# Optimization experiments

Hardware: AMD Instinct MI355X
Metric: run time of the kernel (lower is better)

The kernel has to match this reference:

```python
import math
import jax, jax.numpy as jnp
import numpy as np

B, S, D, H, FF, L = 2, 1024, 1024, 16, 4096, 4
HD = D // H
EPS = 1e-5


def setup_inputs() -> dict:
    key = jax.random.key(0)
    ks = jax.random.split(key, 14)
    sd = 0.02
    inp = {
        "x": jax.random.normal(ks[0], (B, S, D), jnp.float32),
        "mask": jnp.zeros((S, S), jnp.float32),
        "Wqkv": jax.random.normal(ks[1], (L, D, 3 * D), jnp.float32) * sd,
        "bqkv": jnp.zeros((L, 3 * D), jnp.float32),
        "Wo": jax.random.normal(ks[2], (L, D, D), jnp.float32) * sd,
        "bo": jnp.zeros((L, D), jnp.float32),
        "g1": jnp.ones((L, D), jnp.float32),
        "be1": jnp.zeros((L, D), jnp.float32),
        "W1": jax.random.normal(ks[3], (L, D, FF), jnp.float32) * sd,
        "bf1": jnp.zeros((L, FF), jnp.float32),
        "W2": jax.random.normal(ks[4], (L, FF, D), jnp.float32) * sd,
        "bf2": jnp.zeros((L, D), jnp.float32),
        "g2": jnp.ones((L, D), jnp.float32),
        "be2": jnp.zeros((L, D), jnp.float32),
    }
    return inp


def _layer_norm(x, g, b):
    # biased variance, matching the torch LayerNormalization module
    mean = jnp.mean(x, axis=-1, keepdims=True)
    var = jnp.mean((x - mean) ** 2, axis=-1, keepdims=True)
    return g * (x - mean) / jnp.sqrt(var + EPS) + b


def _encoder(x, mask, params):
    inv_sqrt_dk = 1.0 / math.sqrt(HD)

    def step(h, p):
        Wqkv, bqkv, Wo, bo, g1, be1, W1, bf1, W2, bf2, g2, be2 = p
        b, s, d = h.shape
        qkv = h @ Wqkv + bqkv                         # [B,S,3D]
        qkv = qkv.reshape(b, s, H, 3 * HD).transpose(0, 2, 1, 3)  # [B,H,S,3hd]
        q, k, v = jnp.split(qkv, 3, axis=-1)          # each [B,H,S,hd]
        scores = jnp.einsum("bhqd,bhkd->bhqk", q, k) * inv_sqrt_dk + mask
        attn = jax.nn.softmax(scores, axis=-1)
        vals = jnp.einsum("bhqk,bhkd->bhqd", attn, v)
        vals = vals.transpose(0, 2, 1, 3).reshape(b, s, d)
        a = vals @ Wo + bo
        h = _layer_norm(h + a, g1, be1)
        f = jax.nn.relu(h @ W1 + bf1) @ W2 + bf2
        h = _layer_norm(h + f, g2, be2)
        return h, None

    out, _ = jax.lax.scan(step, x, params)
    return out


def reference(x, mask, Wqkv, bqkv, Wo, bo, g1, be1, W1, bf1, W2, bf2, g2, be2):
    params = (Wqkv, bqkv, Wo, bo, g1, be1, W1, bf1, W2, bf2, g2, be2)
    return _encoder(x, mask, params)
```

## Files before the change

kernel.cpp:

```cpp
#include <hip/hip_runtime.h>
#include <hip/hip_bf16.h>
#include <cmath>

typedef __attribute__((ext_vector_type(8))) short short8;
typedef __attribute__((ext_vector_type(4))) float f32x4;

#define EPI_QKV 0
#define EPI_RELU 2
#define EPI_PART 3

__device__ __forceinline__ void gl2lds16(const void* g, void* l) {
  __builtin_amdgcn_global_load_lds(
      (const __attribute__((address_space(1))) unsigned int*)g,
      (__attribute__((address_space(3))) unsigned int*)l, 16, 0, 0);
}

template <int EPI>
__global__ __launch_bounds__(256) void gemm_k(
    const __hip_bfloat16* __restrict__ A, const __hip_bfloat16* __restrict__ WT,
    const float* __restrict__ bias, float* __restrict__ outF,
    __hip_bfloat16* __restrict__ outB, __hip_bfloat16* __restrict__ Qo,
    __hip_bfloat16* __restrict__ Ko, __hip_bfloat16* __restrict__ VTo, int M,
    int N, int K, int P) {
  __shared__ __align__(16) __hip_bfloat16 Alds[128 * 32];
  __shared__ __align__(16) __hip_bfloat16 Blds[128 * 32];
  const int tid = threadIdx.x;
  const int nbn = N >> 7;
  const int npb = (M >> 7) * nbn;
  const int nwg = gridDim.x;
  const int cpx = nwg >> 3;
  const int bid = blockIdx.x;
  const int wg = (bid & 7) * cpx + (bid >> 3);
  const int part = wg / npb;
  const int wgl = wg - part * npb;
  const int bm = wgl / nbn, bn = wgl - bm * nbn;
  const int brow = bm << 7, bcol = bn << 7;
  const int lane = tid & 63;
  const int wid = tid >> 6;
  const int wm = wid >> 1, wn = wid & 1;
  const int lr = lane & 15, lk = lane >> 4;
  const int Kp = K / P;
  const int k0 = part * Kp;

  f32x4 acc[4][4] = {};

  const int srow = tid >> 2;
  const int ssw = (tid >> 3) & 3;
  const int scol = (((tid & 3) ^ ssw) << 3);
  const __hip_bfloat16* aptr = A + (size_t)(brow + srow) * K + scol + k0;
  const __hip_bfloat16* bptr = WT + (size_t)(bcol + srow) * K + scol + k0;
  __hip_bfloat16* la = &Alds[tid * 8];
  __hip_bfloat16* lb = &Blds[tid * 8];
  const size_t K64 = (size_t)64 * K;
  const int fsw = (lr >> 1) & 3;

  for (int kt = 0; kt < Kp; kt += 32) {
    gl2lds16(aptr + kt, la);
    gl2lds16(aptr + K64 + kt, la + 2048);
    gl2lds16(bptr + kt, lb);
    gl2lds16(bptr + K64 + kt, lb + 2048);
    __syncthreads();
    short8 af[4], bf[4];
#pragma unroll
    for (int m = 0; m < 4; ++m)
      af[m] = *(const short8*)&Alds[(wm * 64 + m * 16 + lr) * 32 + ((lk ^ fsw) << 3)];
#pragma unroll
    for (int n = 0; n < 4; ++n)
      bf[n] = *(const short8*)&Blds[(wn * 64 + n * 16 + lr) * 32 + ((lk ^ fsw) << 3)];
#pragma unroll
    for (int m = 0; m < 4; ++m)
#pragma unroll
      for (int n = 0; n < 4; ++n)
        acc[m][n] =
            __builtin_amdgcn_mfma_f32_16x16x32_bf16(af[m], bf[n], acc[m][n], 0, 0, 0);
    __syncthreads();
  }

#pragma unroll
  for (int n = 0; n < 4; ++n) {
    const int c = bcol + wn * 64 + n * 16 + lr;
    float bb = 0.f;
    if constexpr (EPI != EPI_PART) bb = bias[c];
#pragma unroll
    for (int m = 0; m < 4; ++m) {
#pragma unroll
      for (int r = 0; r < 4; ++r) {
        const int row = brow + wm * 64 + m * 16 + lk * 4 + r;
        float v = acc[m][n][r] + bb;
        if constexpr (EPI == EPI_PART) {
          outF[((size_t)part * M + row) * N + c] = v;
        } else if constexpr (EPI == EPI_RELU) {
          outB[(size_t)row * N + c] = __float2bfloat16(fmaxf(v, 0.f));
        } else {
          const int b = row >> 10, s = row & 1023;
          const int hh = c / 192, t = c - hh * 192;
          const size_t base = ((size_t)(b * 16 + hh) * 1024 + s) * 64;
          if (t < 64)
            Qo[base + t] = __float2bfloat16(v);
          else if (t < 128)
            Ko[base + t - 64] = __float2bfloat16(v);
          else
            VTo[((size_t)(b * 16 + hh) * 64 + (t - 128)) * 1024 + s] =
                __float2bfloat16(v);
        }
      }
    }
  }
}

__global__ __launch_bounds__(256) void attn_k(const __hip_bfloat16* __restrict__ Q,
                                              const __hip_bfloat16* __restrict__ Kx,
                                              const __hip_bfloat16* __restrict__ VT,
                                              __hip_bfloat16* __restrict__ O) {
  __shared__ __align__(16) __hip_bfloat16 Plds[4][16][72];
  const int tid = threadIdx.x, lane = tid & 63, w = tid >> 6;
  const int lr = lane & 15, lk = lane >> 4;
  const int bh = blockIdx.y;
  const int q0 = blockIdx.x * 64 + w * 16;
  const __hip_bfloat16* Qb = Q + (size_t)bh * 65536;
  const __hip_bfloat16* Kb = Kx + (size_t)bh * 65536;
  const __hip_bfloat16* Vb = VT + (size_t)bh * 65536;

  short8 aq[2];
#pragma unroll
  for (int ks = 0; ks < 2; ++ks)
    aq[ks] = *(const short8*)(Qb + (size_t)(q0 + lr) * 64 + ks * 32 + lk * 8);

  float mrow[4] = {-INFINITY, -INFINITY, -INFINITY, -INFINITY};
  float lrow[4] = {0.f, 0.f, 0.f, 0.f};
  f32x4 oacc[4] = {};

  for (int kt = 0; kt < 1024; kt += 64) {
    f32x4 sc[4] = {};
#pragma unroll
    for (int nt = 0; nt < 4; ++nt) {
      const __hip_bfloat16* kp = Kb + (size_t)(kt + nt * 16 + lr) * 64 + lk * 8;
      short8 k0 = *(const short8*)kp;
      short8 k1 = *(const short8*)(kp + 32);
      sc[nt] = __builtin_amdgcn_mfma_f32_16x16x32_bf16(aq[0], k0, sc[nt], 0, 0, 0);
      sc[nt] = __builtin_amdgcn_mfma_f32_16x16x32_bf16(aq[1], k1, sc[nt], 0, 0, 0);
    }
#pragma unroll
    for (int r = 0; r < 4; ++r) {
      float mx = fmaxf(fmaxf(sc[0][r], sc[1][r]), fmaxf(sc[2][r], sc[3][r])) * 0.125f;
#pragma unroll
      for (int off = 1; off < 16; off <<= 1) mx = fmaxf(mx, __shfl_xor(mx, off, 64));
      const float mnew = fmaxf(mrow[r], mx);
      const float corr = __expf(mrow[r] - mnew);
      mrow[r] = mnew;
      float rs = 0.f;
#pragma unroll
      for (int nt = 0; nt < 4; ++nt) {
        const float pv = __expf(sc[nt][r] * 0.125f - mnew);
        sc[nt][r] = pv;
        rs += pv;
      }
#pragma unroll
      for (int off = 1; off < 16; off <<= 1) rs += __shfl_xor(rs, off, 64);
      lrow[r] = lrow[r] * corr + rs;
#pragma unroll
      for (int nt = 0; nt < 4; ++nt) oacc[nt][r] *= corr;
    }
#pragma unroll
    for (int nt = 0; nt < 4; ++nt)
#pragma unroll
      for (int r = 0; r < 4; ++r)
        Plds[w][lk * 4 + r][nt * 16 + lr] = __float2bfloat16(sc[nt][r]);
    __syncthreads();
    short8 pa[2];
#pragma unroll
    for (int ks = 0; ks < 2; ++ks)
      pa[ks] = *(const short8*)&Plds[w][lr][ks * 32 + lk * 8];
#pragma unroll
    for (int nt = 0; nt < 4; ++nt) {
      const __hip_bfloat16* vp = Vb + (size_t)(nt * 16 + lr) * 1024 + kt + lk * 8;
      short8 v0 = *(const short8*)vp;
      short8 v1 = *(const short8*)(vp + 32);
      oacc[nt] = __builtin_amdgcn_mfma_f32_16x16x32_bf16(pa[0], v0, oacc[nt], 0, 0, 0);
      oacc[nt] = __builtin_amdgcn_mfma_f32_16x16x32_bf16(pa[1], v1, oacc[nt], 0, 0, 0);
    }
    __syncthreads();
  }

  const int b = bh >> 4, hh = bh & 15;
  float inv[4];
#pragma unroll
  for (int r = 0; r < 4; ++r) inv[r] = 1.f / lrow[r];
#pragma unroll
  for (int nt = 0; nt < 4; ++nt)
#pragma unroll
    for (int r = 0; r < 4; ++r) {
      const int s = q0 + lk * 4 + r;
      O[((size_t)(b * 1024 + s)) * 1024 + hh * 64 + nt * 16 + lr] =
          __float2bfloat16(oacc[nt][r] * inv[r]);
    }
}

__global__ __launch_bounds__(256) void ln_red_k(
    const float* __restrict__ part, const float* __restrict__ resid,
    const float* __restrict__ bias, const float* __restrict__ g,
    const float* __restrict__ be, float* __restrict__ hf,
    __hip_bfloat16* __restrict__ hb, int P) {
  const int row = blockIdx.x, tid = threadIdx.x;
  const size_t MN = (size_t)2048 * 1024;
  float4 v = ((const float4*)(resid + (size_t)row * 1024))[tid];
  const float4 bb = ((const float4*)bias)[tid];
  v.x += bb.x; v.y += bb.y; v.z += bb.z; v.w += bb.w;
#pragma unroll 4
  for (int p = 0; p < P; ++p) {
    const float4 pv = ((const float4*)(part + p * MN + (size_t)row * 1024))[tid];
    v.x += pv.x; v.y += pv.y; v.z += pv.z; v.w += pv.w;
  }
  float s = v.x + v.y + v.z + v.w;
  float q = v.x * v.x + v.y * v.y + v.z * v.z + v.w * v.w;
#pragma unroll
  for (int off = 1; off < 64; off <<= 1) {
    s += __shfl_xor(s, off, 64);
    q += __shfl_xor(q, off, 64);
  }
  __shared__ float ss[4], qs[4];
  const int w = tid >> 6;
  if ((tid & 63) == 0) { ss[w] = s; qs[w] = q; }
  __syncthreads();
  s = ss[0] + ss[1] + ss[2] + ss[3];
  q = qs[0] + qs[1] + qs[2] + qs[3];
  const float mean = s * (1.f / 1024.f);
  const float var = fmaxf(q * (1.f / 1024.f) - mean * mean, 0.f);
  const float rstd = rsqrtf(var + 1e-5f);
  const float4 gv = ((const float4*)g)[tid];
  const float4 bv = ((const float4*)be)[tid];
  float4 o;
  o.x = gv.x * (v.x - mean) * rstd + bv.x;
  o.y = gv.y * (v.y - mean) * rstd + bv.y;
  o.z = gv.z * (v.z - mean) * rstd + bv.z;
  o.w = gv.w * (v.w - mean) * rstd + bv.w;
  ((float4*)(hf + (size_t)row * 1024))[tid] = o;
  __hip_bfloat16* hp = hb + (size_t)row * 1024 + tid * 4;
  hp[0] = __float2bfloat16(o.x);
  hp[1] = __float2bfloat16(o.y);
  hp[2] = __float2bfloat16(o.z);
  hp[3] = __float2bfloat16(o.w);
}

__global__ __launch_bounds__(256) void tconv_k(const float* __restrict__ W,
                                               __hip_bfloat16* __restrict__ WT,
                                               int K, int N) {
  __shared__ __hip_bfloat16 t[64][65];
  const int tid = threadIdx.x;
  const float* src = W + (size_t)blockIdx.z * K * N;
  __hip_bfloat16* dst = WT + (size_t)blockIdx.z * N * K;
  const int n0 = blockIdx.x << 6, k0 = blockIdx.y << 6;
#pragma unroll
  for (int i = tid; i < 1024; i += 256) {
    const int r = i >> 4, c = (i & 15) << 2;
    const float4 v = *(const float4*)(src + (size_t)(k0 + r) * N + n0 + c);
    t[r][c + 0] = __float2bfloat16(v.x);
    t[r][c + 1] = __float2bfloat16(v.y);
    t[r][c + 2] = __float2bfloat16(v.z);
    t[r][c + 3] = __float2bfloat16(v.w);
  }
  __syncthreads();
#pragma unroll
  for (int i = tid; i < 1024; i += 256) {
    const int r = i >> 4, c = (i & 15) << 2;
    __hip_bfloat16* d = dst + (size_t)(n0 + r) * K + k0 + c;
    d[0] = t[c + 0][r];
    d[1] = t[c + 1][r];
    d[2] = t[c + 2][r];
    d[3] = t[c + 3][r];
  }
}

__global__ __launch_bounds__(256) void initx_k(const float* __restrict__ x,
                                               float* __restrict__ hf,
                                               __hip_bfloat16* __restrict__ hb) {
  const int i = blockIdx.x * 256 + threadIdx.x;
  const float4 v = ((const float4*)x)[i];
  ((float4*)hf)[i] = v;
  __hip_bfloat16* hp = hb + (size_t)i * 4;
  hp[0] = __float2bfloat16(v.x);
  hp[1] = __float2bfloat16(v.y);
  hp[2] = __float2bfloat16(v.z);
  hp[3] = __float2bfloat16(v.w);
}

extern "C" void kernel_launch(void* const* d_in, const int* in_sizes, int n_in,
                              void* d_out, int out_size, void* d_ws, size_t ws_size,
                              hipStream_t stream) {
  const float* x = (const float*)d_in[0];
  const float* Wqkv = (const float*)d_in[2];
  const float* bqkv = (const float*)d_in[3];
  const float* Wo = (const float*)d_in[4];
  const float* bo = (const float*)d_in[5];
  const float* g1 = (const float*)d_in[6];
  const float* be1 = (const float*)d_in[7];
  const float* W1 = (const float*)d_in[8];
  const float* bf1 = (const float*)d_in[9];
  const float* W2 = (const float*)d_in[10];
  const float* bf2 = (const float*)d_in[11];
  const float* g2 = (const float*)d_in[12];
  const float* be2 = (const float*)d_in[13];

  char* p = (char*)d_ws;
  auto take = [&](size_t bytes) {
    char* r = p;
    p += (bytes + 255) & ~(size_t)255;
    return r;
  };
  __hip_bfloat16* WqkvT = (__hip_bfloat16*)take(12582912ull * 2);
  __hip_bfloat16* WoT = (__hip_bfloat16*)take(4194304ull * 2);
  __hip_bfloat16* W1T = (__hip_bfloat16*)take(16777216ull * 2);
  __hip_bfloat16* W2T = (__hip_bfloat16*)take(16777216ull * 2);
  float* hf = (float*)take(2097152ull * 4);
  float* partf = (float*)take(4ull * 2097152ull * 4);
  __hip_bfloat16* hb = (__hip_bfloat16*)take(2097152ull * 2);
  __hip_bfloat16* Qb = (__hip_bfloat16*)take(2097152ull * 2);
  __hip_bfloat16* Kb = (__hip_bfloat16*)take(2097152ull * 2);
  __hip_bfloat16* Vb = (__hip_bfloat16*)take(2097152ull * 2);
  __hip_bfloat16* att = (__hip_bfloat16*)take(2097152ull * 2);
  __hip_bfloat16* f1 = (__hip_bfloat16*)take(8388608ull * 2);

  tconv_k<<<dim3(48, 16, 4), 256, 0, stream>>>(Wqkv, WqkvT, 1024, 3072);
  tconv_k<<<dim3(16, 16, 4), 256, 0, stream>>>(Wo, WoT, 1024, 1024);
  tconv_k<<<dim3(64, 16, 4), 256, 0, stream>>>(W1, W1T, 1024, 4096);
  tconv_k<<<dim3(16, 64, 4), 256, 0, stream>>>(W2, W2T, 4096, 1024);
  initx_k<<<2048, 256, 0, stream>>>(x, hf, hb);

  for (int l = 0; l < 4; ++l) {
    gemm_k<EPI_QKV><<<384, 256, 0, stream>>>(
        hb, WqkvT + (size_t)l * 3145728, bqkv + l * 3072, nullptr, nullptr, Qb, Kb,
        Vb, 2048, 3072, 1024, 1);
    attn_k<<<dim3(16, 32), 256, 0, stream>>>(Qb, Kb, Vb, att);
    gemm_k<EPI_PART><<<512, 256, 0, stream>>>(
        att, WoT + (size_t)l * 1048576, nullptr, partf, nullptr, nullptr, nullptr,
        nullptr, 2048, 1024, 1024, 4);
    ln_red_k<<<2048, 256, 0, stream>>>(partf, hf, bo + l * 1024, g1 + l * 1024,
                                       be1 + l * 1024, hf, hb, 4);
    gemm_k<EPI_RELU><<<512, 256, 0, stream>>>(
        hb, W1T + (size_t)l * 4194304, bf1 + l * 4096, nullptr, f1, nullptr, nullptr,
        nullptr, 2048, 4096, 1024, 1);
    gemm_k<EPI_PART><<<512, 256, 0, stream>>>(
        f1, W2T + (size_t)l * 4194304, nullptr, partf, nullptr, nullptr, nullptr,
        nullptr, 2048, 1024, 4096, 4);
    float* lnout = (l == 3) ? (float*)d_out : hf;
    ln_red_k<<<2048, 256, 0, stream>>>(partf, hf, bf2 + l * 1024, g2 + l * 1024,
                                       be2 + l * 1024, lnout, hb, 4);
  }
}
```

Baseline: 1.025 ms.

## Transpose attention MFMA operands so each query row lives in lane columns

Swaps the A/B operands of both attention MFMAs so each lane column holds one query. The softmax row max and sum then need only two cross-lane shuffles, with one m/l per lane instead of four. P is written to LDS as packed 4-element vectors and the block-wide __syncthreads calls are removed, relying on each wave using only its own LDS slice. Output stores also become packed 4-element vector writes. Dropping the barrier assumes wave-local LDS ordering holds within a wavefront, which is fragile if the compiler reorders the LDS write and read.

```diff
diff --git a/kernel.cpp b/kernel.cpp
--- a/kernel.cpp
+++ b/kernel.cpp
@@ -3,6 +3,7 @@
 #include <cmath>
 
 typedef __attribute__((ext_vector_type(8))) short short8;
+typedef __attribute__((ext_vector_type(4))) short short4v;
 typedef __attribute__((ext_vector_type(4))) float f32x4;
 
 #define EPI_QKV 0
@@ -112,7 +113,7 @@
                                               const __hip_bfloat16* __restrict__ Kx,
                                               const __hip_bfloat16* __restrict__ VT,
                                               __hip_bfloat16* __restrict__ O) {
-  __shared__ __align__(16) __hip_bfloat16 Plds[4][16][72];
+  __shared__ __align__(16) __hip_bfloat16 P2[4][16][72];
   const int tid = threadIdx.x, lane = tid & 63, w = tid >> 6;
   const int lr = lane & 15, lk = lane >> 4;
   const int bh = blockIdx.y;
@@ -121,13 +122,12 @@
   const __hip_bfloat16* Kb = Kx + (size_t)bh * 65536;
   const __hip_bfloat16* Vb = VT + (size_t)bh * 65536;
 
-  short8 aq[2];
+  short8 bq[2];
 #pragma unroll
   for (int ks = 0; ks < 2; ++ks)
-    aq[ks] = *(const short8*)(Qb + (size_t)(q0 + lr) * 64 + ks * 32 + lk * 8);
-
-  float mrow[4] = {-INFINITY, -INFINITY, -INFINITY, -INFINITY};
-  float lrow[4] = {0.f, 0.f, 0.f, 0.f};
+    bq[ks] = *(const short8*)(Qb + (size_t)(q0 + lr) * 64 + ks * 32 + lk * 8);
+
+  float m = -INFINITY, l = 0.f;
   f32x4 oacc[4] = {};
 
   for (int kt = 0; kt < 1024; kt += 64) {
@@ -137,63 +137,69 @@
       const __hip_bfloat16* kp = Kb + (size_t)(kt + nt * 16 + lr) * 64 + lk * 8;
       short8 k0 = *(const short8*)kp;
       short8 k1 = *(const short8*)(kp + 32);
-      sc[nt] = __builtin_amdgcn_mfma_f32_16x16x32_bf16(aq[0], k0, sc[nt], 0, 0, 0);
-      sc[nt] = __builtin_amdgcn_mfma_f32_16x16x32_bf16(aq[1], k1, sc[nt], 0, 0, 0);
+      sc[nt] = __builtin_amdgcn_mfma_f32_16x16x32_bf16(k0, bq[0], sc[nt], 0, 0, 0);
+      sc[nt] = __builtin_amdgcn_mfma_f32_16x16x32_bf16(k1, bq[1], sc[nt], 0, 0, 0);
     }
-#pragma unroll
-    for (int r = 0; r < 4; ++r) {
-      float mx = fmaxf(fmaxf(sc[0][r], sc[1][r]), fmaxf(sc[2][r], sc[3][r])) * 0.125f;
-#pragma unroll
-      for (int off = 1; off < 16; off <<= 1) mx = fmaxf(mx, __shfl_xor(mx, off, 64));
-      const float mnew = fmaxf(mrow[r], mx);
-      const float corr = __expf(mrow[r] - mnew);
-      mrow[r] = mnew;
-      float rs = 0.f;
-#pragma unroll
-      for (int nt = 0; nt < 4; ++nt) {
+    float mx = sc[0][0];
+#pragma unroll
+    for (int nt = 0; nt < 4; ++nt)
+#pragma unroll
+      for (int r = 0; r < 4; ++r) mx = fmaxf(mx, sc[nt][r]);
+    mx *= 0.125f;
+    mx = fmaxf(mx, __shfl_xor(mx, 16, 64));
+    mx = fmaxf(mx, __shfl_xor(mx, 32, 64));
+    const float mnew = fmaxf(m, mx);
+    const float corr = __expf(m - mnew);
+    m = mnew;
+    float rs = 0.f;
+#pragma unroll
+    for (int nt = 0; nt < 4; ++nt)
+#pragma unroll
+      for (int r = 0; r < 4; ++r) {
         const float pv = __expf(sc[nt][r] * 0.125f - mnew);
         sc[nt][r] = pv;
         rs += pv;
       }
-#pragma unroll
-      for (int off = 1; off < 16; off <<= 1) rs += __shfl_xor(rs, off, 64);
-      lrow[r] = lrow[r] * corr + rs;
-#pragma unroll
-      for (int nt = 0; nt < 4; ++nt) oacc[nt][r] *= corr;
+    rs += __shfl_xor(rs, 16, 64);
+    rs += __shfl_xor(rs, 32, 64);
+    l = l * corr + rs;
+#pragma unroll
+    for (int dt = 0; dt < 4; ++dt)
+#pragma unroll
+      for (int r = 0; r < 4; ++r) oacc[dt][r] *= corr;
+#pragma unroll
+    for (int nt = 0; nt < 4; ++nt) {
+      short4v pk;
+#pragma unroll
+      for (int r = 0; r < 4; ++r)
+        pk[r] = (short)__bfloat16_as_ushort(__float2bfloat16(sc[nt][r]));
+      *(short4v*)&P2[w][lr][nt * 16 + lk * 4] = pk;
     }
-#pragma unroll
-    for (int nt = 0; nt < 4; ++nt)
-#pragma unroll
-      for (int r = 0; r < 4; ++r)
-        Plds[w][lk * 4 + r][nt * 16 + lr] = __float2bfloat16(sc[nt][r]);
-    __syncthreads();
-    short8 pa[2];
-#pragma unroll
-    for (int ks = 0; ks < 2; ++ks)
-      pa[ks] = *(const short8*)&Plds[w][lr][ks * 32 + lk * 8];
-#pragma unroll
-    for (int nt = 0; nt < 4; ++nt) {
-      const __hip_bfloat16* vp = Vb + (size_t)(nt * 16 + lr) * 1024 + kt + lk * 8;
+    short8 bp[2];
+#pragma unroll
+    for (int kb = 0; kb < 2; ++kb)
+      bp[kb] = *(const short8*)&P2[w][lr][kb * 32 + lk * 8];
+#pragma unroll
+    for (int dt = 0; dt < 4; ++dt) {
+      const __hip_bfloat16* vp = Vb + (size_t)(dt * 16 + lr) * 1024 + kt + lk * 8;
       short8 v0 = *(const short8*)vp;
       short8 v1 = *(const short8*)(vp + 32);
-      oacc[nt] = __builtin_amdgcn_mfma_f32_16x16x32_bf16(pa[0], v0, oacc[nt], 0, 0, 0);
-      oacc[nt] = __builtin_amdgcn_mfma_f32_16x16x32_bf16(pa[1], v1, oacc[nt], 0, 0, 0);
+      oacc[dt] = __builtin_amdgcn_mfma_f32_16x16x32_bf16(v0, bp[0], oacc[dt], 0, 0, 0);
+      oacc[dt] = __builtin_amdgcn_mfma_f32_16x16x32_bf16(v1, bp[1], oacc[dt], 0, 0, 0);
     }
-    __syncthreads();
   }
 
   const int b = bh >> 4, hh = bh & 15;
-  float inv[4];
-#pragma unroll
-  for (int r = 0; r < 4; ++r) inv[r] = 1.f / lrow[r];
-#pragma unroll
-  for (int nt = 0; nt < 4; ++nt)
-#pragma unroll
-    for (int r = 0; r < 4; ++r) {
-      const int s = q0 + lk * 4 + r;
-      O[((size_t)(b * 1024 + s)) * 1024 + hh * 64 + nt * 16 + lr] =
-          __float2bfloat16(oacc[nt][r] * inv[r]);
-    }
+  const float inv = 1.f / l;
+#pragma unroll
+  for (int dt = 0; dt < 4; ++dt) {
+    short4v pk;
+#pragma unroll
+    for (int r = 0; r < 4; ++r)
+      pk[r] = (short)__bfloat16_as_ushort(__float2bfloat16(oacc[dt][r] * inv));
+    *(short4v*)(O + ((size_t)(b * 1024 + q0 + lr)) * 1024 + hh * 64 + dt * 16 +
+                lk * 4) = pk;
+  }
 }
 
 __global__ __launch_bounds__(256) void ln_red_k(
```

Measured after the change: 998.5 us. -2.6%, faster.
